# Kernel optimization log

Hardware: AMD Instinct MI355X
Metric: run time of the kernel (lower is better)

## Reference

```python
import jax, jax.numpy as jnp
import numpy as np

N = 8192
IN_F = 256
OUT_F = 256


def setup_inputs() -> dict:
    key = jax.random.key(0)
    k_v, k_adj, k1, k2, k3, kb = jax.random.split(key, 6)
    stdv = 1.0 / np.sqrt(OUT_F)
    V = jax.random.normal(k_v, (N, IN_F), dtype=jnp.float32)
    adj = jax.random.randint(k_adj, (N, N), 0, 4, dtype=jnp.int32)
    w1 = jax.random.uniform(k1, (IN_F, OUT_F), jnp.float32, -stdv, stdv)
    w2 = jax.random.uniform(k2, (IN_F, OUT_F), jnp.float32, -stdv, stdv)
    w3 = jax.random.uniform(k3, (IN_F, OUT_F), jnp.float32, -stdv, stdv)
    bias = jax.random.uniform(kb, (OUT_F,), jnp.float32, -stdv, stdv)
    return {"V": V, "adj": adj, "w1": w1, "w2": w2, "w3": w3, "bias": bias}


def reference(V, adj, w1, w2, w3, bias):
    # typed relational GCN: for each edge type k in {1,2,3},
    # aggregate (adj==k) @ (V @ wk), then sum and add bias
    o1 = jnp.matmul((adj == 1).astype(jnp.float32), jnp.matmul(V, w1))
    o2 = jnp.matmul((adj == 2).astype(jnp.float32), jnp.matmul(V, w2))
    o3 = jnp.matmul((adj == 3).astype(jnp.float32), jnp.matmul(V, w3))
    return o1 + o2 + o3 + bias
```

## Files before the change

kernel.cpp:

```cpp
#include <hip/hip_runtime.h>

typedef __attribute__((ext_vector_type(4))) float f32x4;
typedef __attribute__((ext_vector_type(16))) float f32x16;
typedef __attribute__((ext_vector_type(4))) unsigned short u16x4;
typedef __attribute__((ext_vector_type(4))) int i32x4;
typedef __attribute__((ext_vector_type(8))) __bf16 bf16x8;

union FragAB {
  u16x4 u[2];
  i32x4 v;
  bf16x8 f;
};

static __device__ __forceinline__ unsigned short f2bf(float x) {
  union { float f; unsigned u; } v;
  v.f = x;
  unsigned r = v.u + 0x7FFFu + ((v.u >> 16) & 1u);
  return (unsigned short)(r >> 16);
}
static __device__ __forceinline__ float b2f(unsigned short u) {
  union { unsigned u; float f; } v;
  v.u = ((unsigned)u) << 16;
  return v.f;
}

#define NN 8192

__global__ __launch_bounds__(256) void k_bias(const float* __restrict__ bias,
                                              float* __restrict__ out) {
  out[(size_t)blockIdx.x * 256 + threadIdx.x] = bias[threadIdx.x];
}

__global__ __launch_bounds__(256) void k_transform(
    const float* __restrict__ V, const float* __restrict__ w1,
    const float* __restrict__ w2, const float* __restrict__ w3,
    unsigned short* __restrict__ Bp) {
  int bx = blockIdx.x;
  int rb = bx & 63;
  int nb = bx >> 6;
  const float* W = (nb < 4) ? w1 : (nb < 8) ? w2 : w3;
  int nc0 = (nb & 3) * 64;
  int tid = threadIdx.x;
  int lane = tid & 63;
  int wv = tid >> 6;
  int wm = wv >> 1, wn = wv & 1;
  int q = lane >> 4, l16 = lane & 15;

  __shared__ unsigned short tA[128][36];
  __shared__ unsigned short tB[64][36];

  f32x4 acc[4][2];
#pragma unroll
  for (int i = 0; i < 4; i++)
#pragma unroll
    for (int j = 0; j < 2; j++) acc[i][j] = (f32x4)0.0f;

  for (int kk = 0; kk < 256; kk += 32) {
    {
      int r = tid >> 1, c0 = (tid & 1) * 16;
      const float* src = V + (size_t)(rb * 128 + r) * 256 + kk + c0;
      f32x4 f0 = *(const f32x4*)(src + 0);
      f32x4 f1 = *(const f32x4*)(src + 4);
      f32x4 f2 = *(const f32x4*)(src + 8);
      f32x4 f3 = *(const f32x4*)(src + 12);
      unsigned short* d = &tA[r][c0];
      d[0] = f2bf(f0.x);  d[1] = f2bf(f0.y);  d[2] = f2bf(f0.z);  d[3] = f2bf(f0.w);
      d[4] = f2bf(f1.x);  d[5] = f2bf(f1.y);  d[6] = f2bf(f1.z);  d[7] = f2bf(f1.w);
      d[8] = f2bf(f2.x);  d[9] = f2bf(f2.y);  d[10] = f2bf(f2.z); d[11] = f2bf(f2.w);
      d[12] = f2bf(f3.x); d[13] = f2bf(f3.y); d[14] = f2bf(f3.z); d[15] = f2bf(f3.w);
    }
    {
      int r = tid >> 3, c0 = (tid & 7) * 8;
      const float* src = W + (size_t)(kk + r) * 256 + nc0 + c0;
      f32x4 g0 = *(const f32x4*)(src);
      f32x4 g1 = *(const f32x4*)(src + 4);
      tB[c0 + 0][r] = f2bf(g0.x); tB[c0 + 1][r] = f2bf(g0.y);
      tB[c0 + 2][r] = f2bf(g0.z); tB[c0 + 3][r] = f2bf(g0.w);
      tB[c0 + 4][r] = f2bf(g1.x); tB[c0 + 5][r] = f2bf(g1.y);
      tB[c0 + 6][r] = f2bf(g1.z); tB[c0 + 7][r] = f2bf(g1.w);
    }
    __syncthreads();
    FragAB af[4], bf[2];
#pragma unroll
    for (int mt = 0; mt < 4; mt++) {
      const unsigned short* p = &tA[wm * 64 + mt * 16 + l16][q * 8];
      af[mt].u[0] = *(const u16x4*)p;
      af[mt].u[1] = *(const u16x4*)(p + 4);
    }
#pragma unroll
    for (int nt = 0; nt < 2; nt++) {
      const unsigned short* p = &tB[wn * 32 + nt * 16 + l16][q * 8];
      bf[nt].u[0] = *(const u16x4*)p;
      bf[nt].u[1] = *(const u16x4*)(p + 4);
    }
#pragma unroll
    for (int mt = 0; mt < 4; mt++)
#pragma unroll
      for (int nt = 0; nt < 2; nt++)
        acc[mt][nt] = __builtin_amdgcn_mfma_f32_16x16x32_bf16(
            af[mt].f, bf[nt].f, acc[mt][nt], 0, 0, 0);
    __syncthreads();
  }
  int ty = nb >> 2;
#pragma unroll
  for (int mt = 0; mt < 4; mt++)
#pragma unroll
    for (int nt = 0; nt < 2; nt++) {
      int n = (nb & 3) * 64 + wn * 32 + nt * 16 + l16;
      int j0 = rb * 128 + wm * 64 + mt * 16 + q * 4;
      u16x4 hv;
      hv.x = f2bf(acc[mt][nt].x);
      hv.y = f2bf(acc[mt][nt].y);
      hv.z = f2bf(acc[mt][nt].z);
      hv.w = f2bf(acc[mt][nt].w);
      size_t idx = (size_t)ty * 2097152 + (size_t)(j0 >> 4) * 4096 + n * 16 + (j0 & 15);
      *(u16x4*)(Bp + idx) = hv;
    }
}

__global__ __launch_bounds__(256) void k_fix(unsigned short* __restrict__ Bp) {
  size_t i = ((size_t)blockIdx.x * 256 + threadIdx.x) * 8;
  union { i32x4 v; unsigned short s[8]; } a, b, c, r;
  a.v = *(const i32x4*)(Bp + i);
  b.v = *(const i32x4*)(Bp + 2097152 + i);
  c.v = *(const i32x4*)(Bp + 4194304 + i);
#pragma unroll
  for (int e = 0; e < 8; e++)
    r.s[e] = f2bf(b2f(c.s[e]) - b2f(a.s[e]) - b2f(b.s[e]));
  *(i32x4*)(Bp + 4194304 + i) = r.v;
}

__global__ __launch_bounds__(256) void k_pack(const int* __restrict__ adj,
                                              unsigned* __restrict__ P) {
  int bx = blockIdx.x;
  int rowblk = bx >> 3, ks = bx & 7;
  int t = threadIdx.x;
  int r0 = rowblk * 64;
  __shared__ unsigned hal[64][129];

  for (int p = 0; p < 32; p++) {
    int rl = p * 2 + (t >> 7);
    int o = t & 127;
    const int* src = adj + (size_t)(r0 + rl) * NN + ks * 1024 + o * 8;
    i32x4 v0 = *(const i32x4*)src;
    i32x4 v1 = *(const i32x4*)(src + 4);
    unsigned b = (unsigned)(v0.x & 3) | ((unsigned)(v0.y & 3) << 2) |
                 ((unsigned)(v0.z & 3) << 4) | ((unsigned)(v0.w & 3) << 6) |
                 ((unsigned)(v1.x & 3) << 8) | ((unsigned)(v1.y & 3) << 10) |
                 ((unsigned)(v1.z & 3) << 12) | ((unsigned)(v1.w & 3) << 14);
    hal[rl][o] = b;
  }
  __syncthreads();
  for (int i = 0; i < 16; i++) {
    int oi = i * 256 + t;
    int row = oi & 63, sq = oi >> 6;
    int s = sq >> 1, q = sq & 1;
    unsigned lo = hal[row][s * 4 + q];
    unsigned hi = hal[row][s * 4 + 2 + q];
    P[((size_t)(ks * 32 + s) * 2 + q) * 8192 + r0 + row] = lo | (hi << 16);
  }
}

static __device__ __forceinline__ void expand2(unsigned bits, FragAB& fA,
                                               FragAB& fB) {
  unsigned short a[8], b[8];
#pragma unroll
  for (int e = 0; e < 8; e++) {
    a[e] = (bits & (1u << (2 * e))) ? 0x3F80 : 0;
    b[e] = (bits & (2u << (2 * e))) ? 0x3F80 : 0;
  }
  fA.u[0] = u16x4{a[0], a[1], a[2], a[3]};
  fA.u[1] = u16x4{a[4], a[5], a[6], a[7]};
  fB.u[0] = u16x4{b[0], b[1], b[2], b[3]};
  fB.u[1] = u16x4{b[4], b[5], b[6], b[7]};
}

__global__ __launch_bounds__(256) void k_agg(const unsigned* __restrict__ P,
                                             const unsigned short* __restrict__ Bp,
                                             float* __restrict__ out) {
  int bx = blockIdx.x;
  int ks = bx & 7, rb = bx >> 3;
  int tid = threadIdx.x, lane = tid & 63;
  int wv = tid >> 6;
  int q = lane >> 5, l32 = lane & 31;

  f32x16 acc[2][2];
  acc[0][0] = (f32x16)0.0f;
  acc[0][1] = (f32x16)0.0f;
  acc[1][0] = (f32x16)0.0f;
  acc[1][1] = (f32x16)0.0f;

  const unsigned* pp = P + ((size_t)ks * 64 + q) * 8192 + rb * 64 + l32;

  const unsigned short* bb[3][2];
#pragma unroll
  for (int ty = 0; ty < 3; ty++)
#pragma unroll
    for (int nt = 0; nt < 2; nt++) {
      int n = wv * 64 + nt * 32 + l32;
      bb[ty][nt] = Bp + (size_t)ty * 2097152 + (size_t)ks * 262144 + n * 16 + q * 8;
    }

  unsigned pk0 = pp[0], pk1 = pp[32];

  for (int s = 0; s < 32; s++) {
    FragAB bv[2][3][2];
    size_t soff = (size_t)s * 8192;
#pragma unroll
    for (int kh = 0; kh < 2; kh++)
#pragma unroll
      for (int ty = 0; ty < 3; ty++)
#pragma unroll
        for (int nt = 0; nt < 2; nt++)
          bv[kh][ty][nt].v = *(const i32x4*)(bb[ty][nt] + soff + kh * 4096);
    unsigned npk0 = 0, npk1 = 0;
    if (s < 31) {
      npk0 = pp[(s + 1) * 16384];
      npk1 = pp[(s + 1) * 16384 + 32];
    }
#pragma unroll
    for (int mt = 0; mt < 2; mt++) {
      unsigned pw = mt ? pk1 : pk0;
#pragma unroll
      for (int kh = 0; kh < 2; kh++) {
        unsigned bits = (pw >> (kh * 16)) & 0xFFFFu;
        FragAB fA, fB, fC;
        expand2(bits, fA, fB);
        fC.v = fA.v & fB.v;
        acc[mt][0] = __builtin_amdgcn_mfma_f32_32x32x16_bf16(
            fA.f, bv[kh][0][0].f, acc[mt][0], 0, 0, 0);
        acc[mt][1] = __builtin_amdgcn_mfma_f32_32x32x16_bf16(
            fA.f, bv[kh][0][1].f, acc[mt][1], 0, 0, 0);
        acc[mt][0] = __builtin_amdgcn_mfma_f32_32x32x16_bf16(
            fB.f, bv[kh][1][0].f, acc[mt][0], 0, 0, 0);
        acc[mt][1] = __builtin_amdgcn_mfma_f32_32x32x16_bf16(
            fB.f, bv[kh][1][1].f, acc[mt][1], 0, 0, 0);
        acc[mt][0] = __builtin_amdgcn_mfma_f32_32x32x16_bf16(
            fC.f, bv[kh][2][0].f, acc[mt][0], 0, 0, 0);
        acc[mt][1] = __builtin_amdgcn_mfma_f32_32x32x16_bf16(
            fC.f, bv[kh][2][1].f, acc[mt][1], 0, 0, 0);
      }
    }
    pk0 = npk0;
    pk1 = npk1;
  }

#pragma unroll
  for (int mt = 0; mt < 2; mt++)
#pragma unroll
    for (int nt = 0; nt < 2; nt++) {
      int colbase = wv * 64 + nt * 32 + l32;
      int rowb = rb * 64 + mt * 32 + 4 * q;
#pragma unroll
      for (int r = 0; r < 16; r++) {
        int row = rowb + (r & 3) + 8 * (r >> 2);
        atomicAdd(out + (size_t)row * 256 + colbase, acc[mt][nt][r]);
      }
    }
}

extern "C" void kernel_launch(void* const* d_in, const int* in_sizes, int n_in,
                              void* d_out, int out_size, void* d_ws,
                              size_t ws_size, hipStream_t stream) {
  const float* V = (const float*)d_in[0];
  const int* adj = (const int*)d_in[1];
  const float* w1 = (const float*)d_in[2];
  const float* w2 = (const float*)d_in[3];
  const float* w3 = (const float*)d_in[4];
  const float* bias = (const float*)d_in[5];
  float* out = (float*)d_out;
  unsigned short* Bp = (unsigned short*)d_ws;
  unsigned* P = (unsigned*)((char*)d_ws + 12582912);

  k_bias<<<dim3(NN), dim3(256), 0, stream>>>(bias, out);
  k_pack<<<dim3(1024), dim3(256), 0, stream>>>(adj, P);
  k_transform<<<dim3(768), dim3(256), 0, stream>>>(V, w1, w2, w3, Bp);
  k_fix<<<dim3(1024), dim3(256), 0, stream>>>(Bp);
  k_agg<<<dim3(1024), dim3(256), 0, stream>>>(P, Bp, out);
}
```

Baseline: 523.1 us.

## Fold weight fix into transform, split pack rows, double agg row tile

After: 541.2 us. +3.5%, slower.

```diff
diff --git a/kernel.cpp b/kernel.cpp
--- a/kernel.cpp
+++ b/kernel.cpp
@@ -17,11 +17,6 @@
   v.f = x;
   unsigned r = v.u + 0x7FFFu + ((v.u >> 16) & 1u);
   return (unsigned short)(r >> 16);
-}
-static __device__ __forceinline__ float b2f(unsigned short u) {
-  union { unsigned u; float f; } v;
-  v.u = ((unsigned)u) << 16;
-  return v.f;
 }
 
 #define NN 8192
@@ -38,7 +33,6 @@
   int bx = blockIdx.x;
   int rb = bx & 63;
   int nb = bx >> 6;
-  const float* W = (nb < 4) ? w1 : (nb < 8) ? w2 : w3;
   int nc0 = (nb & 3) * 64;
   int tid = threadIdx.x;
   int lane = tid & 63;
@@ -70,14 +64,26 @@
       d[12] = f2bf(f3.x); d[13] = f2bf(f3.y); d[14] = f2bf(f3.z); d[15] = f2bf(f3.w);
     }
     {
-      int r = tid >> 3, c0 = (tid & 7) * 8;
-      const float* src = W + (size_t)(kk + r) * 256 + nc0 + c0;
-      f32x4 g0 = *(const f32x4*)(src);
-      f32x4 g1 = *(const f32x4*)(src + 4);
-      tB[c0 + 0][r] = f2bf(g0.x); tB[c0 + 1][r] = f2bf(g0.y);
-      tB[c0 + 2][r] = f2bf(g0.z); tB[c0 + 3][r] = f2bf(g0.w);
-      tB[c0 + 4][r] = f2bf(g1.x); tB[c0 + 5][r] = f2bf(g1.y);
-      tB[c0 + 6][r] = f2bf(g1.z); tB[c0 + 7][r] = f2bf(g1.w);
+      int r = tid >> 3, cg = (tid & 7) * 8;
+      size_t off = (size_t)(kk + r) * 256 + nc0 + cg;
+      f32x4 g0, g1;
+      if (nb < 4) {
+        g0 = *(const f32x4*)(w1 + off);
+        g1 = *(const f32x4*)(w1 + off + 4);
+      } else if (nb < 8) {
+        g0 = *(const f32x4*)(w2 + off);
+        g1 = *(const f32x4*)(w2 + off + 4);
+      } else {
+        f32x4 a0 = *(const f32x4*)(w1 + off), a1 = *(const f32x4*)(w1 + off + 4);
+        f32x4 b0 = *(const f32x4*)(w2 + off), b1 = *(const f32x4*)(w2 + off + 4);
+        f32x4 d0 = *(const f32x4*)(w3 + off), d1 = *(const f32x4*)(w3 + off + 4);
+        g0 = d0 - a0 - b0;
+        g1 = d1 - a1 - b1;
+      }
+      tB[cg + 0][r] = f2bf(g0.x); tB[cg + 1][r] = f2bf(g0.y);
+      tB[cg + 2][r] = f2bf(g0.z); tB[cg + 3][r] = f2bf(g0.w);
+      tB[cg + 4][r] = f2bf(g1.x); tB[cg + 5][r] = f2bf(g1.y);
+      tB[cg + 6][r] = f2bf(g1.z); tB[cg + 7][r] = f2bf(g1.w);
     }
     __syncthreads();
     FragAB af[4], bf[2];
@@ -118,42 +124,36 @@
     }
 }
 
-__global__ __launch_bounds__(256) void k_fix(unsigned short* __restrict__ Bp) {
-  size_t i = ((size_t)blockIdx.x * 256 + threadIdx.x) * 8;
-  union { i32x4 v; unsigned short s[8]; } a, b, c, r;
-  a.v = *(const i32x4*)(Bp + i);
-  b.v = *(const i32x4*)(Bp + 2097152 + i);
-  c.v = *(const i32x4*)(Bp + 4194304 + i);
-#pragma unroll
-  for (int e = 0; e < 8; e++)
-    r.s[e] = f2bf(b2f(c.s[e]) - b2f(a.s[e]) - b2f(b.s[e]));
-  *(i32x4*)(Bp + 4194304 + i) = r.v;
-}
-
 __global__ __launch_bounds__(256) void k_pack(const int* __restrict__ adj,
                                               unsigned* __restrict__ P) {
   int bx = blockIdx.x;
   int rowblk = bx >> 3, ks = bx & 7;
   int t = threadIdx.x;
-  int r0 = rowblk * 64;
-  __shared__ unsigned hal[64][129];
-
-  for (int p = 0; p < 32; p++) {
-    int rl = p * 2 + (t >> 7);
-    int o = t & 127;
-    const int* src = adj + (size_t)(r0 + rl) * NN + ks * 1024 + o * 8;
-    i32x4 v0 = *(const i32x4*)src;
-    i32x4 v1 = *(const i32x4*)(src + 4);
-    unsigned b = (unsigned)(v0.x & 3) | ((unsigned)(v0.y & 3) << 2) |
-                 ((unsigned)(v0.z & 3) << 4) | ((unsigned)(v0.w & 3) << 6) |
-                 ((unsigned)(v1.x & 3) << 8) | ((unsigned)(v1.y & 3) << 10) |
-                 ((unsigned)(v1.z & 3) << 12) | ((unsigned)(v1.w & 3) << 14);
-    hal[rl][o] = b;
+  int r0 = rowblk * 32;
+  __shared__ unsigned hal[32][129];
+
+  int rl = t >> 7;
+  int o = t & 127;
+  const int* src0 = adj + (size_t)(r0 + rl) * NN + ks * 1024 + o * 8;
+  i32x4 v0 = *(const i32x4*)src0;
+  i32x4 v1 = *(const i32x4*)(src0 + 4);
+  for (int p = 0; p < 16; p++) {
+    i32x4 u0 = v0, u1 = v1;
+    if (p < 15) {
+      const int* s = src0 + (size_t)(p + 1) * 2 * NN;
+      v0 = *(const i32x4*)s;
+      v1 = *(const i32x4*)(s + 4);
+    }
+    unsigned b = (unsigned)(u0.x & 3) | ((unsigned)(u0.y & 3) << 2) |
+                 ((unsigned)(u0.z & 3) << 4) | ((unsigned)(u0.w & 3) << 6) |
+                 ((unsigned)(u1.x & 3) << 8) | ((unsigned)(u1.y & 3) << 10) |
+                 ((unsigned)(u1.z & 3) << 12) | ((unsigned)(u1.w & 3) << 14);
+    hal[p * 2 + rl][o] = b;
   }
   __syncthreads();
-  for (int i = 0; i < 16; i++) {
+  for (int i = 0; i < 8; i++) {
     int oi = i * 256 + t;
-    int row = oi & 63, sq = oi >> 6;
+    int row = oi & 31, sq = oi >> 5;
     int s = sq >> 1, q = sq & 1;
     unsigned lo = hal[row][s * 4 + q];
     unsigned hi = hal[row][s * 4 + 2 + q];
@@ -175,22 +175,23 @@
   fB.u[1] = u16x4{b[4], b[5], b[6], b[7]};
 }
 
-__global__ __launch_bounds__(256) void k_agg(const unsigned* __restrict__ P,
-                                             const unsigned short* __restrict__ Bp,
-                                             float* __restrict__ out) {
+__global__ __launch_bounds__(256, 2) void k_agg(const unsigned* __restrict__ P,
+                                                const unsigned short* __restrict__ Bp,
+                                                float* __restrict__ out) {
   int bx = blockIdx.x;
   int ks = bx & 7, rb = bx >> 3;
   int tid = threadIdx.x, lane = tid & 63;
   int wv = tid >> 6;
   int q = lane >> 5, l32 = lane & 31;
 
-  f32x16 acc[2][2];
-  acc[0][0] = (f32x16)0.0f;
-  acc[0][1] = (f32x16)0.0f;
-  acc[1][0] = (f32x16)0.0f;
-  acc[1][1] = (f32x16)0.0f;
-
-  const unsigned* pp = P + ((size_t)ks * 64 + q) * 8192 + rb * 64 + l32;
+  f32x16 acc[4][2];
+#pragma unroll
+  for (int mt = 0; mt < 4; mt++) {
+    acc[mt][0] = (f32x16)0.0f;
+    acc[mt][1] = (f32x16)0.0f;
+  }
+
+  const unsigned* pp = P + ((size_t)ks * 64 + q) * 8192 + rb * 128 + l32;
 
   const unsigned short* bb[3][2];
 #pragma unroll
@@ -201,7 +202,9 @@
       bb[ty][nt] = Bp + (size_t)ty * 2097152 + (size_t)ks * 262144 + n * 16 + q * 8;
     }
 
-  unsigned pk0 = pp[0], pk1 = pp[32];
+  unsigned pk[4], npk[4];
+#pragma unroll
+  for (int mt = 0; mt < 4; mt++) pk[mt] = pp[mt * 32];
 
   for (int s = 0; s < 32; s++) {
     FragAB bv[2][3][2];
@@ -213,17 +216,16 @@
 #pragma unroll
         for (int nt = 0; nt < 2; nt++)
           bv[kh][ty][nt].v = *(const i32x4*)(bb[ty][nt] + soff + kh * 4096);
-    unsigned npk0 = 0, npk1 = 0;
     if (s < 31) {
-      npk0 = pp[(s + 1) * 16384];
-      npk1 = pp[(s + 1) * 16384 + 32];
-    }
-#pragma unroll
-    for (int mt = 0; mt < 2; mt++) {
-      unsigned pw = mt ? pk1 : pk0;
+#pragma unroll
+      for (int mt = 0; mt < 4; mt++)
+        npk[mt] = pp[(size_t)(s + 1) * 16384 + mt * 32];
+    }
+#pragma unroll
+    for (int mt = 0; mt < 4; mt++) {
 #pragma unroll
       for (int kh = 0; kh < 2; kh++) {
-        unsigned bits = (pw >> (kh * 16)) & 0xFFFFu;
+        unsigned bits = (pk[mt] >> (kh * 16)) & 0xFFFFu;
         FragAB fA, fB, fC;
         expand2(bits, fA, fB);
         fC.v = fA.v & fB.v;
@@ -241,16 +243,16 @@
             fC.f, bv[kh][2][1].f, acc[mt][1], 0, 0, 0);
       }
     }
-    pk0 = npk0;
-    pk1 = npk1;
-  }
-
-#pragma unroll
-  for (int mt = 0; mt < 2; mt++)
+#pragma unroll
+    for (int mt = 0; mt < 4; mt++) pk[mt] = npk[mt];
+  }
+
+#pragma unroll
+  for (int mt = 0; mt < 4; mt++)
 #pragma unroll
     for (int nt = 0; nt < 2; nt++) {
       int colbase = wv * 64 + nt * 32 + l32;
-      int rowb = rb * 64 + mt * 32 + 4 * q;
+      int rowb = rb * 128 + mt * 32 + 4 * q;
 #pragma unroll
       for (int r = 0; r < 16; r++) {
         int row = rowb + (r & 3) + 8 * (r >> 2);
@@ -273,8 +275,7 @@
   unsigned* P = (unsigned*)((char*)d_ws + 12582912);
 
   k_bias<<<dim3(NN), dim3(256), 0, stream>>>(bias, out);
-  k_pack<<<dim3(1024), dim3(256), 0, stream>>>(adj, P);
+  k_pack<<<dim3(2048), dim3(256), 0, stream>>>(adj, P);
   k_transform<<<dim3(768), dim3(256), 0, stream>>>(V, w1, w2, w3, Bp);
-  k_fix<<<dim3(1024), dim3(256), 0, stream>>>(Bp);
-  k_agg<<<dim3(1024), dim3(256), 0, stream>>>(P, Bp, out);
-}
+  k_agg<<<dim3(512), dim3(256), 0, stream>>>(P, Bp, out);
+}
```
